# Performance work log

Measured on AMD Instinct MI355X. Metric: run time of the kernel, lower is better.

Reference implementation:

```python
import jax, jax.numpy as jnp
import numpy as np

N_NODES = 50000
N_EDGES = 800000
D_FEAT = 128


def setup_inputs() -> dict:
    key = jax.random.key(0)
    k1, k2, k3 = jax.random.split(key, 3)
    x = jax.random.normal(k1, (N_NODES, D_FEAT), dtype=jnp.float32)
    edge_index = jax.random.randint(k2, (2, N_EDGES), 0, N_NODES, dtype=jnp.int64)
    eps = jnp.zeros((1,), dtype=jnp.float32)  # trainable eps, init 0
    p = jax.random.uniform(k3, (1,), dtype=jnp.float32, minval=-1.0, maxval=1.0)
    return {"x": x, "edge_index": edge_index, "eps": eps, "p": p}


def reference(x, edge_index, eps, p):
    # x: [N, d]; edge_index: [2, E] with (row, col)
    row, col = edge_index[0], edge_index[1]
    n = x.shape[0]

    # symmetric-ish GCN norm (degree computed over col only, as in source)
    deg = jax.ops.segment_sum(jnp.ones_like(col, dtype=x.dtype), col, num_segments=n)
    deg_inv_sqrt = jnp.where(deg > 0, deg ** -0.5, 0.0)
    norm = deg_inv_sqrt[row] * deg_inv_sqrt[col]  # [E]

    # nonlinear aggregation branch
    pp = jax.nn.sigmoid(p) * 2.0  # scalar in (0, 2)
    scale = pp * x  # [N, d]
    softmax = jnp.exp(scale - scale.max())  # global-max-stabilized exp

    sm_col = softmax[col]  # [E, d] gather
    deg_div = jax.ops.segment_sum(sm_col * norm[:, None], row, num_segments=n)  # [N, d]
    weights = sm_col / (deg_div[row] + 1e-6)  # [E, d]

    agg = jax.ops.segment_sum(weights * x[col] * norm[:, None], row, num_segments=n)  # [N, d]
    out = agg + (1.0 + eps) * x
    return out
```

## Files before the change

kernel.cpp:

```cpp
#include <hip/hip_runtime.h>
#include <hip/hip_fp16.h>
#include <math.h>

#define N_NODES 50000
#define N_EDGES 800000
#define D_FEAT 128

#define BSHIFT 6
#define BNODES 64
#define NBUCK ((N_NODES + BNODES - 1) / BNODES)
#define BCAP 1280
#define SLOT_CAP 64

#define PART_BLOCKS 256
#define PART_CHUNK (N_EDGES / PART_BLOCKS)

typedef __attribute__((ext_vector_type(4))) _Float16 half4;

__global__ void __launch_bounds__(256) k_cvtmax(const float* __restrict__ x,
                                                half4* __restrict__ x16,
                                                float* __restrict__ partials) {
    const float4* x4 = (const float4*)x;
    const int total4 = N_NODES * D_FEAT / 4;
    float m = -INFINITY;
    for (int i = blockIdx.x * blockDim.x + threadIdx.x; i < total4; i += gridDim.x * blockDim.x) {
        float4 v = x4[i];
        m = fmaxf(m, fmaxf(fmaxf(v.x, v.y), fmaxf(v.z, v.w)));
        half4 h;
        h.x = (_Float16)v.x; h.y = (_Float16)v.y; h.z = (_Float16)v.z; h.w = (_Float16)v.w;
        x16[i] = h;
    }
    for (int off = 32; off > 0; off >>= 1)
        m = fmaxf(m, __shfl_down(m, off, 64));
    __shared__ float smem[4];
    int lane = threadIdx.x & 63, wid = threadIdx.x >> 6;
    if (lane == 0) smem[wid] = m;
    __syncthreads();
    if (threadIdx.x == 0)
        partials[blockIdx.x] = fmaxf(fmaxf(smem[0], smem[1]), fmaxf(smem[2], smem[3]));
}

__global__ void __launch_bounds__(256) k_max2(const float* __restrict__ partials,
                                              float* __restrict__ maxval) {
    float m = fmaxf(partials[threadIdx.x], partials[threadIdx.x + 256]);
    for (int off = 32; off > 0; off >>= 1)
        m = fmaxf(m, __shfl_down(m, off, 64));
    __shared__ float smem[4];
    int lane = threadIdx.x & 63, wid = threadIdx.x >> 6;
    if (lane == 0) smem[wid] = m;
    __syncthreads();
    if (threadIdx.x == 0)
        maxval[0] = fmaxf(fmaxf(smem[0], smem[1]), fmaxf(smem[2], smem[3]));
}

__global__ void __launch_bounds__(512) k_part(const int* __restrict__ row,
                                              const int* __restrict__ col,
                                              int* __restrict__ gcur_row,
                                              int* __restrict__ gcur_col,
                                              int2* __restrict__ be_row,
                                              int* __restrict__ be_col) {
    __shared__ int h_row[NBUCK];
    __shared__ int h_col[NBUCK];
    int e0 = blockIdx.x * PART_CHUNK;
    for (int i = threadIdx.x; i < NBUCK; i += 512) { h_row[i] = 0; h_col[i] = 0; }
    __syncthreads();
    for (int e = e0 + threadIdx.x; e < e0 + PART_CHUNK; e += 512) {
        atomicAdd(&h_row[row[e] >> BSHIFT], 1);
        atomicAdd(&h_col[col[e] >> BSHIFT], 1);
    }
    __syncthreads();
    for (int i = threadIdx.x; i < NBUCK; i += 512) {
        int base_r = atomicAdd(&gcur_row[i], h_row[i]);
        h_row[i] = i * BCAP + base_r;
        int base_c = atomicAdd(&gcur_col[i], h_col[i]);
        h_col[i] = i * BCAP + base_c;
    }
    __syncthreads();
    for (int e = e0 + threadIdx.x; e < e0 + PART_CHUNK; e += 512) {
        int r = row[e], c = col[e];
        int pr = atomicAdd(&h_row[r >> BSHIFT], 1);
        if (pr < (r >> BSHIFT) * BCAP + BCAP) be_row[pr] = make_int2(r, c);
        int pc = atomicAdd(&h_col[c >> BSHIFT], 1);
        if (pc < (c >> BSHIFT) * BCAP + BCAP) be_col[pc] = c;
    }
}

__global__ void __launch_bounds__(256) k_degcol(const int* __restrict__ gcur_col,
                                                const int* __restrict__ be_col,
                                                float* __restrict__ dis) {
    __shared__ int h[BNODES];
    int b = blockIdx.x;
    if (threadIdx.x < BNODES) h[threadIdx.x] = 0;
    __syncthreads();
    int cnt = min(gcur_col[b], BCAP);
    int base = b * BCAP;
    for (int k = threadIdx.x; k < cnt; k += 256)
        atomicAdd(&h[be_col[base + k] & (BNODES - 1)], 1);
    __syncthreads();
    if (threadIdx.x < BNODES) {
        int n = (b << BSHIFT) + threadIdx.x;
        if (n < N_NODES) {
            int d = h[threadIdx.x];
            dis[n] = (d > 0) ? rsqrtf((float)d) : 0.0f;
        }
    }
}

__global__ void __launch_bounds__(512) k_agg(const half4* __restrict__ x16,
                                             const float* __restrict__ x,
                                             const int* __restrict__ gcur_row,
                                             const int2* __restrict__ be_row,
                                             const float* __restrict__ dis,
                                             const float* __restrict__ maxval,
                                             const float* __restrict__ eps_p,
                                             const float* __restrict__ p_p,
                                             float* __restrict__ out) {
    __shared__ int s_cnt[BNODES];
    __shared__ int s_slot[BNODES][SLOT_CAP];
    __shared__ float s_dis[BNODES][SLOT_CAP];
    int b = blockIdx.x;
    if (threadIdx.x < BNODES) s_cnt[threadIdx.x] = 0;
    __syncthreads();
    int ecnt = min(gcur_row[b], BCAP);
    int base = b * BCAP;
    for (int k = threadIdx.x; k < ecnt; k += 512) {
        int2 e = be_row[base + k];
        int ln = e.x & (BNODES - 1);
        int pos = atomicAdd(&s_cnt[ln], 1);
        if (pos < SLOT_CAP) {
            s_slot[ln][pos] = e.y;
            s_dis[ln][pos] = dis[e.y];
        }
    }
    __syncthreads();

    int g = threadIdx.x >> 5;
    int t = threadIdx.x & 31;
    float pp = 2.0f / (1.0f + __expf(-p_p[0]));
    float M  = pp * maxval[0];
    float ke = 1.0f + eps_p[0];
    const float4* x4 = (const float4*)x;

    for (int ln = g; ln < BNODES; ln += 16) {
        int n = (b << BSHIFT) + ln;
        if (n >= N_NODES) continue;
        int cnt = min(s_cnt[ln], SLOT_CAP);
        float dn = dis[n];
        float4 S = make_float4(0.f, 0.f, 0.f, 0.f);
        float4 T = make_float4(0.f, 0.f, 0.f, 0.f);
        #pragma unroll 4
        for (int j = 0; j < cnt; ++j) {
            int c = s_slot[ln][j];
            float nr = dn * s_dis[ln][j];
            half4 hv = x16[c * 32 + t];
            float x0 = (float)hv.x, x1 = (float)hv.y, x2 = (float)hv.z, x3 = (float)hv.w;
            float e0 = __expf(fmaf(pp, x0, -M));
            float e1 = __expf(fmaf(pp, x1, -M));
            float e2 = __expf(fmaf(pp, x2, -M));
            float e3 = __expf(fmaf(pp, x3, -M));
            float w0 = nr * e0, w1 = nr * e1, w2 = nr * e2, w3 = nr * e3;
            S.x += w0; S.y += w1; S.z += w2; S.w += w3;
            T.x = fmaf(w0, x0, T.x);
            T.y = fmaf(w1, x1, T.y);
            T.z = fmaf(w2, x2, T.z);
            T.w = fmaf(w3, x3, T.w);
        }
        float4 xn = x4[n * 32 + t];
        float4 o;
        o.x = T.x / (S.x + 1e-6f) + ke * xn.x;
        o.y = T.y / (S.y + 1e-6f) + ke * xn.y;
        o.z = T.z / (S.z + 1e-6f) + ke * xn.z;
        o.w = T.w / (S.w + 1e-6f) + ke * xn.w;
        ((float4*)out)[n * 32 + t] = o;
    }
}

extern "C" void kernel_launch(void* const* d_in, const int* in_sizes, int n_in,
                              void* d_out, int out_size, void* d_ws, size_t ws_size,
                              hipStream_t stream) {
    const float* x   = (const float*)d_in[0];
    const int*   ei  = (const int*)d_in[1];
    const float* eps = (const float*)d_in[2];
    const float* p   = (const float*)d_in[3];
    float* out = (float*)d_out;

    const int* row = ei;
    const int* col = ei + N_EDGES;

    char* ws = (char*)d_ws;
    int*   gcur_row = (int*)ws;
    int*   gcur_col = (int*)(ws + 4 * NBUCK);
    float* maxval   = (float*)(ws + 4 * 2 * NBUCK);
    float* partials = (float*)(ws + 4 * (2 * NBUCK + 1));
    float* dis      = (float*)(ws + 4 * (2 * NBUCK + 1 + 512));
    size_t off = 4 * (size_t)(2 * NBUCK + 1 + 512 + N_NODES);
    off = (off + 15) & ~(size_t)15;
    half4* x16      = (half4*)(ws + off);
    off += (size_t)N_NODES * D_FEAT * 2;
    int*   be_col   = (int*)(ws + off);
    off += (size_t)NBUCK * BCAP * 4;
    int2*  be_row   = (int2*)(ws + off);

    hipMemsetAsync(ws, 0, 4 * 2 * NBUCK, stream);

    k_cvtmax<<<512, 256, 0, stream>>>(x, x16, partials);
    k_max2<<<1, 256, 0, stream>>>(partials, maxval);
    k_part<<<PART_BLOCKS, 512, 0, stream>>>(row, col, gcur_row, gcur_col, be_row, be_col);
    k_degcol<<<NBUCK, 256, 0, stream>>>(gcur_col, be_col, dis);
    k_agg<<<NBUCK, 512, 0, stream>>>(x16, x, gcur_row, be_row, dis, maxval, eps, p, out);
}
```

Measured before the change: 169.7 us.

## Fold max reduction and degree count into partition kernel, shrink buckets

Removes the separate max-reduction and column-bucketing/degree kernels. The final max is computed inside block 0 of the partition kernel, and in-degree is counted with global atomics on a per-node array. The aggregation kernel now computes rsqrt of degree on the fly, uses exp2/rcp intrinsics, and runs smaller 32-node buckets with 256-thread blocks for more blocks. This trades two kernel launches and the col bucket traffic for 800k scattered global atomics and a larger memset.

```diff
diff --git a/kernel.cpp b/kernel.cpp
--- a/kernel.cpp
+++ b/kernel.cpp
@@ -6,16 +6,27 @@
 #define N_EDGES 800000
 #define D_FEAT 128
 
-#define BSHIFT 6
-#define BNODES 64
+#define BSHIFT 5
+#define BNODES 32
 #define NBUCK ((N_NODES + BNODES - 1) / BNODES)
-#define BCAP 1280
+#define BCAP 768
 #define SLOT_CAP 64
 
 #define PART_BLOCKS 256
 #define PART_CHUNK (N_EDGES / PART_BLOCKS)
 
 typedef __attribute__((ext_vector_type(4))) _Float16 half4;
+
+#if __has_builtin(__builtin_amdgcn_exp2f)
+#define EXP2F(a) __builtin_amdgcn_exp2f(a)
+#else
+#define EXP2F(a) exp2f(a)
+#endif
+#if __has_builtin(__builtin_amdgcn_rcpf)
+#define RCPF(a) __builtin_amdgcn_rcpf(a)
+#else
+#define RCPF(a) (1.0f / (a))
+#endif
 
 __global__ void __launch_bounds__(256) k_cvtmax(const float* __restrict__ x,
                                                 half4* __restrict__ x16,
@@ -40,124 +51,101 @@
         partials[blockIdx.x] = fmaxf(fmaxf(smem[0], smem[1]), fmaxf(smem[2], smem[3]));
 }
 
-__global__ void __launch_bounds__(256) k_max2(const float* __restrict__ partials,
-                                              float* __restrict__ maxval) {
-    float m = fmaxf(partials[threadIdx.x], partials[threadIdx.x + 256]);
-    for (int off = 32; off > 0; off >>= 1)
-        m = fmaxf(m, __shfl_down(m, off, 64));
-    __shared__ float smem[4];
-    int lane = threadIdx.x & 63, wid = threadIdx.x >> 6;
-    if (lane == 0) smem[wid] = m;
-    __syncthreads();
-    if (threadIdx.x == 0)
-        maxval[0] = fmaxf(fmaxf(smem[0], smem[1]), fmaxf(smem[2], smem[3]));
-}
-
 __global__ void __launch_bounds__(512) k_part(const int* __restrict__ row,
                                               const int* __restrict__ col,
                                               int* __restrict__ gcur_row,
-                                              int* __restrict__ gcur_col,
+                                              int* __restrict__ deg,
                                               int2* __restrict__ be_row,
-                                              int* __restrict__ be_col) {
+                                              const float* __restrict__ partials,
+                                              float* __restrict__ maxval) {
     __shared__ int h_row[NBUCK];
-    __shared__ int h_col[NBUCK];
+    __shared__ float sm8[8];
+    if (blockIdx.x == 0) {
+        float m = partials[threadIdx.x];
+        for (int off = 32; off > 0; off >>= 1)
+            m = fmaxf(m, __shfl_down(m, off, 64));
+        if ((threadIdx.x & 63) == 0) sm8[threadIdx.x >> 6] = m;
+    }
+    for (int i = threadIdx.x; i < NBUCK; i += 512) h_row[i] = 0;
+    __syncthreads();
+    if (blockIdx.x == 0 && threadIdx.x == 0) {
+        float m = sm8[0];
+        #pragma unroll
+        for (int i = 1; i < 8; ++i) m = fmaxf(m, sm8[i]);
+        maxval[0] = m;
+    }
     int e0 = blockIdx.x * PART_CHUNK;
-    for (int i = threadIdx.x; i < NBUCK; i += 512) { h_row[i] = 0; h_col[i] = 0; }
-    __syncthreads();
-    for (int e = e0 + threadIdx.x; e < e0 + PART_CHUNK; e += 512) {
+    for (int e = e0 + threadIdx.x; e < e0 + PART_CHUNK; e += 512)
         atomicAdd(&h_row[row[e] >> BSHIFT], 1);
-        atomicAdd(&h_col[col[e] >> BSHIFT], 1);
-    }
     __syncthreads();
     for (int i = threadIdx.x; i < NBUCK; i += 512) {
         int base_r = atomicAdd(&gcur_row[i], h_row[i]);
         h_row[i] = i * BCAP + base_r;
-        int base_c = atomicAdd(&gcur_col[i], h_col[i]);
-        h_col[i] = i * BCAP + base_c;
     }
     __syncthreads();
     for (int e = e0 + threadIdx.x; e < e0 + PART_CHUNK; e += 512) {
         int r = row[e], c = col[e];
+        atomicAdd(&deg[c], 1);
         int pr = atomicAdd(&h_row[r >> BSHIFT], 1);
         if (pr < (r >> BSHIFT) * BCAP + BCAP) be_row[pr] = make_int2(r, c);
-        int pc = atomicAdd(&h_col[c >> BSHIFT], 1);
-        if (pc < (c >> BSHIFT) * BCAP + BCAP) be_col[pc] = c;
     }
 }
 
-__global__ void __launch_bounds__(256) k_degcol(const int* __restrict__ gcur_col,
-                                                const int* __restrict__ be_col,
-                                                float* __restrict__ dis) {
-    __shared__ int h[BNODES];
-    int b = blockIdx.x;
-    if (threadIdx.x < BNODES) h[threadIdx.x] = 0;
-    __syncthreads();
-    int cnt = min(gcur_col[b], BCAP);
-    int base = b * BCAP;
-    for (int k = threadIdx.x; k < cnt; k += 256)
-        atomicAdd(&h[be_col[base + k] & (BNODES - 1)], 1);
-    __syncthreads();
-    if (threadIdx.x < BNODES) {
-        int n = (b << BSHIFT) + threadIdx.x;
-        if (n < N_NODES) {
-            int d = h[threadIdx.x];
-            dis[n] = (d > 0) ? rsqrtf((float)d) : 0.0f;
-        }
-    }
-}
-
-__global__ void __launch_bounds__(512) k_agg(const half4* __restrict__ x16,
+__global__ void __launch_bounds__(256) k_agg(const half4* __restrict__ x16,
                                              const float* __restrict__ x,
                                              const int* __restrict__ gcur_row,
                                              const int2* __restrict__ be_row,
-                                             const float* __restrict__ dis,
+                                             const int* __restrict__ deg,
                                              const float* __restrict__ maxval,
                                              const float* __restrict__ eps_p,
                                              const float* __restrict__ p_p,
                                              float* __restrict__ out) {
     __shared__ int s_cnt[BNODES];
     __shared__ int s_slot[BNODES][SLOT_CAP];
-    __shared__ float s_dis[BNODES][SLOT_CAP];
+    __shared__ float s_disv[BNODES][SLOT_CAP];
     int b = blockIdx.x;
     if (threadIdx.x < BNODES) s_cnt[threadIdx.x] = 0;
     __syncthreads();
     int ecnt = min(gcur_row[b], BCAP);
     int base = b * BCAP;
-    for (int k = threadIdx.x; k < ecnt; k += 512) {
+    for (int k = threadIdx.x; k < ecnt; k += 256) {
         int2 e = be_row[base + k];
         int ln = e.x & (BNODES - 1);
         int pos = atomicAdd(&s_cnt[ln], 1);
         if (pos < SLOT_CAP) {
             s_slot[ln][pos] = e.y;
-            s_dis[ln][pos] = dis[e.y];
+            s_disv[ln][pos] = rsqrtf((float)deg[e.y]);
         }
     }
     __syncthreads();
 
     int g = threadIdx.x >> 5;
     int t = threadIdx.x & 31;
+    const float L2E = 1.44269504088896f;
     float pp = 2.0f / (1.0f + __expf(-p_p[0]));
-    float M  = pp * maxval[0];
-    float ke = 1.0f + eps_p[0];
+    float ppl = pp * L2E;
+    float Ml  = pp * maxval[0] * L2E;
+    float ke  = 1.0f + eps_p[0];
     const float4* x4 = (const float4*)x;
 
-    for (int ln = g; ln < BNODES; ln += 16) {
+    for (int ln = g; ln < BNODES; ln += 8) {
         int n = (b << BSHIFT) + ln;
         if (n >= N_NODES) continue;
         int cnt = min(s_cnt[ln], SLOT_CAP);
-        float dn = dis[n];
+        int dni = deg[n];
+        float dn = (dni > 0) ? rsqrtf((float)dni) : 0.0f;
         float4 S = make_float4(0.f, 0.f, 0.f, 0.f);
         float4 T = make_float4(0.f, 0.f, 0.f, 0.f);
         #pragma unroll 4
         for (int j = 0; j < cnt; ++j) {
             int c = s_slot[ln][j];
-            float nr = dn * s_dis[ln][j];
+            float nr = dn * s_disv[ln][j];
             half4 hv = x16[c * 32 + t];
             float x0 = (float)hv.x, x1 = (float)hv.y, x2 = (float)hv.z, x3 = (float)hv.w;
-            float e0 = __expf(fmaf(pp, x0, -M));
-            float e1 = __expf(fmaf(pp, x1, -M));
-            float e2 = __expf(fmaf(pp, x2, -M));
-            float e3 = __expf(fmaf(pp, x3, -M));
+            float e0 = EXP2F(fmaf(ppl, x0, -Ml));
+            float e1 = EXP2F(fmaf(ppl, x1, -Ml));
+            float e2 = EXP2F(fmaf(ppl, x2, -Ml));
+            float e3 = EXP2F(fmaf(ppl, x3, -Ml));
             float w0 = nr * e0, w1 = nr * e1, w2 = nr * e2, w3 = nr * e3;
             S.x += w0; S.y += w1; S.z += w2; S.w += w3;
             T.x = fmaf(w0, x0, T.x);
@@ -167,10 +155,10 @@
         }
         float4 xn = x4[n * 32 + t];
         float4 o;
-        o.x = T.x / (S.x + 1e-6f) + ke * xn.x;
-        o.y = T.y / (S.y + 1e-6f) + ke * xn.y;
-        o.z = T.z / (S.z + 1e-6f) + ke * xn.z;
-        o.w = T.w / (S.w + 1e-6f) + ke * xn.w;
+        o.x = T.x * RCPF(S.x + 1e-6f) + ke * xn.x;
+        o.y = T.y * RCPF(S.y + 1e-6f) + ke * xn.y;
+        o.z = T.z * RCPF(S.z + 1e-6f) + ke * xn.z;
+        o.w = T.w * RCPF(S.w + 1e-6f) + ke * xn.w;
         ((float4*)out)[n * 32 + t] = o;
     }
 }
@@ -189,23 +177,18 @@
 
     char* ws = (char*)d_ws;
     int*   gcur_row = (int*)ws;
-    int*   gcur_col = (int*)(ws + 4 * NBUCK);
-    float* maxval   = (float*)(ws + 4 * 2 * NBUCK);
-    float* partials = (float*)(ws + 4 * (2 * NBUCK + 1));
-    float* dis      = (float*)(ws + 4 * (2 * NBUCK + 1 + 512));
-    size_t off = 4 * (size_t)(2 * NBUCK + 1 + 512 + N_NODES);
+    int*   deg      = (int*)(ws + 4 * NBUCK);
+    float* maxval   = (float*)(ws + 4 * (NBUCK + N_NODES));
+    float* partials = (float*)(ws + 4 * (NBUCK + N_NODES + 1));
+    size_t off = 4 * (size_t)(NBUCK + N_NODES + 1 + 512);
     off = (off + 15) & ~(size_t)15;
     half4* x16      = (half4*)(ws + off);
     off += (size_t)N_NODES * D_FEAT * 2;
-    int*   be_col   = (int*)(ws + off);
-    off += (size_t)NBUCK * BCAP * 4;
     int2*  be_row   = (int2*)(ws + off);
 
-    hipMemsetAsync(ws, 0, 4 * 2 * NBUCK, stream);
+    hipMemsetAsync(ws, 0, 4 * (NBUCK + N_NODES), stream);
 
     k_cvtmax<<<512, 256, 0, stream>>>(x, x16, partials);
-    k_max2<<<1, 256, 0, stream>>>(partials, maxval);
-    k_part<<<PART_BLOCKS, 512, 0, stream>>>(row, col, gcur_row, gcur_col, be_row, be_col);
-    k_degcol<<<NBUCK, 256, 0, stream>>>(gcur_col, be_col, dis);
-    k_agg<<<NBUCK, 512, 0, stream>>>(x16, x, gcur_row, be_row, dis, maxval, eps, p, out);
+    k_part<<<PART_BLOCKS, 512, 0, stream>>>(row, col, gcur_row, deg, be_row, partials, maxval);
+    k_agg<<<NBUCK, 256, 0, stream>>>(x16, x, gcur_row, be_row, deg, maxval, eps, p, out);
 }
```

New measurement: 179.9 us. 1.06x slower.
